# Optimization experiments

Measured on AMD Instinct MI355X. Metric: run time of the kernel, lower is better.

## Reference

```python
import jax, jax.numpy as jnp
import numpy as np

NUM_EXPERT = 16
IN_DIM = 1024
OUT_DIM = 3072
TOTAL_TOKENS = 16384  # tokens pre-grouped by expert, contiguous blocks


def setup_inputs() -> dict:
    key = jax.random.key(0)
    k1, k2, k3 = jax.random.split(key, 3)
    inp = jax.random.normal(k1, (TOTAL_TOKENS, IN_DIM), dtype=jnp.float32)
    # per-expert token counts (sum == TOTAL_TOKENS); even split here
    fwd_expert_count = jnp.full((NUM_EXPERT,), TOTAL_TOKENS // NUM_EXPERT, dtype=jnp.int64)
    scale = 1.0 / np.sqrt(IN_DIM)
    weight = jax.random.normal(k2, (NUM_EXPERT, OUT_DIM, IN_DIM), dtype=jnp.float32) * scale
    bias = jax.random.normal(k3, (NUM_EXPERT, OUT_DIM), dtype=jnp.float32) * scale
    return {"inp": inp, "fwd_expert_count": fwd_expert_count, "weight": weight, "bias": bias}


def reference(inp, fwd_expert_count, weight, bias):
    # Grouped GEMM: token block e (size fwd_expert_count[e]) uses expert e's
    # weight: y = x @ W_e^T + b_e.  Tokens are contiguous per expert, so
    # expert id per token = repeat(arange(E), counts).
    T = inp.shape[0]
    E = weight.shape[0]
    expert_id = jnp.repeat(jnp.arange(E), fwd_expert_count, total_repeat_length=T)  # [T]
    out = jnp.zeros((T, weight.shape[1]), dtype=inp.dtype)
    # small fixed structural loop over experts (E=16); each iter is a dense GEMM
    for e in range(E):
        ye = inp @ weight[e].T + bias[e]  # [T, out_dim]
        out = jnp.where((expert_id == e)[:, None], ye, out)
    return out
```

## Files before the change

### kernel.cpp

```cpp
#include <hip/hip_runtime.h>

typedef __attribute__((ext_vector_type(8))) _Float16 f16x8;
typedef __attribute__((ext_vector_type(2))) __fp16   fp16x2;
typedef __attribute__((ext_vector_type(4))) float    f32x4;

#define TT 16384
#define KD 1024
#define ND 3072
#define NE 16
#define ASZ (TT * KD)
#define WSZ (NE * ND * KD)
#define NEED_WS ((size_t)(ASZ + WSZ) * 2)

#define BM 256
#define BN 256
#define BK 64
#define NSTEP (KD / BK)
#define ROWB (BK * 2)

#define BAR() __builtin_amdgcn_s_barrier()
#define WAIT_VM(n) asm volatile("s_waitcnt vmcnt(" #n ")" ::: "memory")

__device__ __forceinline__ int swz(int row, int kbyte) {
    return row * ROWB + (kbyte ^ ((row & 7) << 4));
}

__device__ __forceinline__ int find_expert(const void* cntp, int row0) {
    const int* w = (const int*)cntp;
    int oddsum = 0;
    #pragma unroll
    for (int i = 1; i < 16; i += 2) oddsum |= w[i];
    int e = 0;
    long long cum = 0;
    if (oddsum == 0) {
        const long long* c = (const long long*)cntp;
        #pragma unroll
        for (int i = 0; i < NE; ++i) { if ((long long)row0 >= cum) e = i; cum += c[i]; }
    } else {
        #pragma unroll
        for (int i = 0; i < NE; ++i) { if ((long long)row0 >= cum) e = i; cum += w[i]; }
    }
    return e;
}

__device__ __forceinline__ void gl16(const void* g, void* l) {
    __builtin_amdgcn_global_load_lds(
        (const __attribute__((address_space(1))) unsigned int*)g,
        (__attribute__((address_space(3))) unsigned int*)l, 16, 0, 0);
}

__global__ __launch_bounds__(256) void cvt_kernel(const float* __restrict__ A,
                                                  const float* __restrict__ W,
                                                  _Float16* __restrict__ dst) {
    size_t i = ((size_t)blockIdx.x * 256 + threadIdx.x) * 8;
    const float* src = (i < (size_t)ASZ) ? (A + i) : (W + (i - ASZ));
    f32x4 v0 = *(const f32x4*)src;
    f32x4 v1 = *(const f32x4*)(src + 4);
    f16x8 h;
    h[0] = (_Float16)v0[0]; h[1] = (_Float16)v0[1];
    h[2] = (_Float16)v0[2]; h[3] = (_Float16)v0[3];
    h[4] = (_Float16)v1[0]; h[5] = (_Float16)v1[1];
    h[6] = (_Float16)v1[2]; h[7] = (_Float16)v1[3];
    *(f16x8*)(dst + i) = h;
}

__launch_bounds__(512, 2)
__global__ void gemm16(const _Float16* __restrict__ A16,
                       const void* __restrict__ cnt,
                       const _Float16* __restrict__ W16,
                       const float* __restrict__ bias,
                       float* __restrict__ Y) {
    __shared__ __align__(16) char lds[2][2][BM * ROWB];

    const int nwg = gridDim.x;
    const int bid0 = blockIdx.x;
    const int wgid = (bid0 & 7) * (nwg >> 3) + (bid0 >> 3);

    const int mt = wgid / (ND / BN);
    const int nt = wgid % (ND / BN);
    const int row0 = mt * BM;
    const int col0 = nt * BN;

    const int e = find_expert(cnt, row0);
    const _Float16* We = W16 + (size_t)e * ND * KD;

    const int tid = threadIdx.x;
    const int l = tid & 63;
    const int w = tid >> 6;
    const int wr = w >> 2;
    const int wc = w & 3;
    const int lr = l & 15;
    const int lk = l >> 4;

    const int laneoff = ((l & 7) * 16) ^ ((l >> 3) << 4);
    const char* gA = (const char*)A16 +
                     (size_t)(row0 + w * 32 + (l >> 3)) * (KD * 2) + laneoff;
    const char* gB = (const char*)We +
                     (size_t)(col0 + w * 32 + (l >> 3)) * (KD * 2) + laneoff;

    auto issue = [&](int t, int buf) {
        const char* a = gA + t * 128;
        const char* b = gB + t * 128;
        char* la = &lds[buf][0][w * 4096];
        char* lb = &lds[buf][1][w * 4096];
        #pragma unroll
        for (int i = 0; i < 4; ++i) {
            gl16(a + i * (8 * KD * 2), la + i * 1024);
            gl16(b + i * (8 * KD * 2), lb + i * 1024);
        }
    };

    f32x4 acc[8][4] = {};

    auto compute = [&](const char* As, const char* Bs) {
        #pragma unroll
        for (int kk = 0; kk < 2; ++kk) {
            f16x8 af[8], bf[4];
            #pragma unroll
            for (int m = 0; m < 8; ++m) {
                int r = wr * 128 + m * 16 + lr;
                af[m] = *(const f16x8*)&As[swz(r, kk * 64 + lk * 16)];
            }
            #pragma unroll
            for (int n = 0; n < 4; ++n) {
                int r = wc * 64 + n * 16 + lr;
                bf[n] = *(const f16x8*)&Bs[swz(r, kk * 64 + lk * 16)];
            }
            __builtin_amdgcn_s_setprio(1);
            #pragma unroll
            for (int m = 0; m < 8; ++m)
                #pragma unroll
                for (int n = 0; n < 4; ++n)
                    acc[m][n] = __builtin_amdgcn_mfma_f32_16x16x32_f16(
                        af[m], bf[n], acc[m][n], 0, 0, 0);
            __builtin_amdgcn_s_setprio(0);
        }
    };

    issue(0, 0);
    issue(1, 1);
    WAIT_VM(8);
    BAR();

    for (int t = 0; t < NSTEP; ++t) {
        const int buf = t & 1;
        compute(lds[buf][0], lds[buf][1]);
        BAR();
        if (t + 2 < NSTEP) {
            issue(t + 2, buf);
            WAIT_VM(8);
            BAR();
        } else if (t + 1 < NSTEP) {
            WAIT_VM(0);
            BAR();
        }
    }

    const int cb = col0 + wc * 64;
    const int rb0_ = row0 + wr * 128;
    float bv[4];
    #pragma unroll
    for (int n = 0; n < 4; ++n) bv[n] = bias[(size_t)e * ND + cb + n * 16 + lr];
    #pragma unroll
    for (int m = 0; m < 8; ++m) {
        #pragma unroll
        for (int j = 0; j < 4; ++j) {
            int r = rb0_ + m * 16 + lk * 4 + j;
            float* yp = Y + (size_t)r * ND + cb + lr;
            #pragma unroll
            for (int n = 0; n < 4; ++n)
                yp[n * 16] = acc[m][n][j] + bv[n];
        }
    }
}

__launch_bounds__(512, 2)
__global__ void fallback_gemm(const float* __restrict__ A,
                              const void* __restrict__ cnt,
                              const float* __restrict__ W,
                              const float* __restrict__ bias,
                              float* __restrict__ Y) {
    __shared__ __align__(16) char ldsbuf[2][2][BM * ROWB];

    const int nwg = gridDim.x;
    const int bid0 = blockIdx.x;
    const int wgid = (bid0 & 7) * (nwg >> 3) + (bid0 >> 3);

    const int mt = wgid / (ND / BN);
    const int nt = wgid % (ND / BN);
    const int row0 = mt * BM;
    const int col0 = nt * BN;

    const int e = find_expert(cnt, row0);
    const float* We = W + (size_t)e * ND * KD;

    const int tid = threadIdx.x;
    const int lane = tid & 63;
    const int w = tid >> 6;
    const int wr = w >> 2;
    const int wc = w & 3;
    const int lr = lane & 15;
    const int lk = lane >> 4;

    int soff[4];
    size_t aoff[4], boff[4];
    #pragma unroll
    for (int c = 0; c < 4; ++c) {
        int q = c * 512 + tid;
        int r = q >> 3;
        int kb = (q & 7) * 8;
        soff[c] = swz(r, kb * 2);
        aoff[c] = (size_t)(row0 + r) * KD + kb;
        boff[c] = (size_t)(col0 + r) * KD + kb;
    }

    f32x4 ra[4][2], rb[4][2];

    auto load_regs = [&](int ks) {
        const int k0 = ks * BK;
        #pragma unroll
        for (int c = 0; c < 4; ++c) {
            const float* ap = A + aoff[c] + k0;
            ra[c][0] = *(const f32x4*)ap;
            ra[c][1] = *(const f32x4*)(ap + 4);
            const float* bp = We + boff[c] + k0;
            rb[c][0] = *(const f32x4*)bp;
            rb[c][1] = *(const f32x4*)(bp + 4);
        }
    };

    auto write_lds = [&](int buf) {
        #pragma unroll
        for (int c = 0; c < 4; ++c) {
            union { f16x8 v; fp16x2 h[4]; } ua, ub;
            ua.h[0] = __builtin_amdgcn_cvt_pkrtz(ra[c][0][0], ra[c][0][1]);
            ua.h[1] = __builtin_amdgcn_cvt_pkrtz(ra[c][0][2], ra[c][0][3]);
            ua.h[2] = __builtin_amdgcn_cvt_pkrtz(ra[c][1][0], ra[c][1][1]);
            ua.h[3] = __builtin_amdgcn_cvt_pkrtz(ra[c][1][2], ra[c][1][3]);
            ub.h[0] = __builtin_amdgcn_cvt_pkrtz(rb[c][0][0], rb[c][0][1]);
            ub.h[1] = __builtin_amdgcn_cvt_pkrtz(rb[c][0][2], rb[c][0][3]);
            ub.h[2] = __builtin_amdgcn_cvt_pkrtz(rb[c][1][0], rb[c][1][1]);
            ub.h[3] = __builtin_amdgcn_cvt_pkrtz(rb[c][1][2], rb[c][1][3]);
            *(f16x8*)&ldsbuf[buf][0][soff[c]] = ua.v;
            *(f16x8*)&ldsbuf[buf][1][soff[c]] = ub.v;
        }
    };

    f32x4 acc[8][4] = {};

    auto compute = [&](const char* As, const char* Bs) {
        #pragma unroll
        for (int kk = 0; kk < 2; ++kk) {
            f16x8 af[8], bf[4];
            #pragma unroll
            for (int m = 0; m < 8; ++m) {
                int r = wr * 128 + m * 16 + lr;
                af[m] = *(const f16x8*)&As[swz(r, kk * 64 + lk * 16)];
            }
            #pragma unroll
            for (int n = 0; n < 4; ++n) {
                int r = wc * 64 + n * 16 + lr;
                bf[n] = *(const f16x8*)&Bs[swz(r, kk * 64 + lk * 16)];
            }
            #pragma unroll
            for (int m = 0; m < 8; ++m)
                #pragma unroll
                for (int n = 0; n < 4; ++n)
                    acc[m][n] = __builtin_amdgcn_mfma_f32_16x16x32_f16(
                        af[m], bf[n], acc[m][n], 0, 0, 0);
        }
    };

    load_regs(0);
    write_lds(0);
    __syncthreads();

    for (int t = 0; t < NSTEP; ++t) {
        const int buf = t & 1;
        if (t + 1 < NSTEP) load_regs(t + 1);
        compute(ldsbuf[buf][0], ldsbuf[buf][1]);
        __syncthreads();
        if (t + 1 < NSTEP) write_lds(buf ^ 1);
        __syncthreads();
    }

    const int cb = col0 + wc * 64;
    const int rb0_ = row0 + wr * 128;
    float bv[4];
    #pragma unroll
    for (int n = 0; n < 4; ++n) bv[n] = bias[(size_t)e * ND + cb + n * 16 + lr];
    #pragma unroll
    for (int m = 0; m < 8; ++m) {
        #pragma unroll
        for (int j = 0; j < 4; ++j) {
            int r = rb0_ + m * 16 + lk * 4 + j;
            float* yp = Y + (size_t)r * ND + cb + lr;
            #pragma unroll
            for (int n = 0; n < 4; ++n)
                yp[n * 16] = acc[m][n][j] + bv[n];
        }
    }
}

extern "C" void kernel_launch(void* const* d_in, const int* in_sizes, int n_in,
                              void* d_out, int out_size, void* d_ws, size_t ws_size,
                              hipStream_t stream) {
    const float* inp  = (const float*)d_in[0];
    const void*  cnt  = d_in[1];
    const float* wgt  = (const float*)d_in[2];
    const float* bias = (const float*)d_in[3];
    float* out = (float*)d_out;

    dim3 grid((TT / BM) * (ND / BN));
    dim3 block(512);

    if (ws_size >= NEED_WS) {
        _Float16* ws16 = (_Float16*)d_ws;
        cvt_kernel<<<dim3((ASZ + WSZ) / (8 * 256)), dim3(256), 0, stream>>>(inp, wgt, ws16);
        gemm16<<<grid, block, 0, stream>>>(ws16, cnt, ws16 + ASZ, bias, out);
    } else {
        fallback_gemm<<<grid, block, 0, stream>>>(inp, cnt, wgt, bias, out);
    }
}
```

Before: 205.9 us.

## Split per-tile compute into four barrier-synchronized phases with one-step prefetch

Each K tile's MFMA work is now split into four quadrant phases. Each phase loads its own A/B fragments from LDS, then hits a barrier, runs its MFMAs at raised priority, and hits another barrier, so waves move in lockstep and LDS reads alternate with math across the workgroup. Prefetch changes from two tiles ahead to one: the next tile's global-to-LDS loads are issued just before computing the current tile, with a single barrier per iteration. This adds many barriers per step and leaves less time to hide load latency, in exchange for the hoped-for better interleaving of LDS traffic and MFMA across waves.

```diff
diff --git a/kernel.cpp b/kernel.cpp
--- a/kernel.cpp
+++ b/kernel.cpp
@@ -64,6 +64,37 @@
     *(f16x8*)(dst + i) = h;
 }
 
+#define PHASE(As, Bs, MH, NH) do {                                          \
+    f16x8 af[2][4], bf[2][2];                                               \
+    _Pragma("unroll")                                                       \
+    for (int kk = 0; kk < 2; ++kk) {                                        \
+        _Pragma("unroll")                                                   \
+        for (int m = 0; m < 4; ++m) {                                       \
+            int r = wr * 128 + ((MH) * 4 + m) * 16 + lr;                    \
+            af[kk][m] = *(const f16x8*)&(As)[swz(r, kk * 64 + lk * 16)];    \
+        }                                                                   \
+        _Pragma("unroll")                                                   \
+        for (int n = 0; n < 2; ++n) {                                       \
+            int r = wc * 64 + ((NH) * 2 + n) * 16 + lr;                     \
+            bf[kk][n] = *(const f16x8*)&(Bs)[swz(r, kk * 64 + lk * 16)];    \
+        }                                                                   \
+    }                                                                       \
+    __builtin_amdgcn_s_barrier();                                           \
+    __builtin_amdgcn_s_setprio(1);                                          \
+    _Pragma("unroll")                                                       \
+    for (int kk = 0; kk < 2; ++kk)                                          \
+        _Pragma("unroll")                                                   \
+        for (int m = 0; m < 4; ++m)                                         \
+            _Pragma("unroll")                                               \
+            for (int n = 0; n < 2; ++n)                                     \
+                acc[(MH) * 4 + m][(NH) * 2 + n] =                           \
+                    __builtin_amdgcn_mfma_f32_16x16x32_f16(                 \
+                        af[kk][m], bf[kk][n],                               \
+                        acc[(MH) * 4 + m][(NH) * 2 + n], 0, 0, 0);          \
+    __builtin_amdgcn_s_setprio(0);                                          \
+    __builtin_amdgcn_s_barrier();                                           \
+} while (0)
+
 __launch_bounds__(512, 2)
 __global__ void gemm16(const _Float16* __restrict__ A16,
                        const void* __restrict__ cnt,
@@ -112,48 +143,24 @@
 
     f32x4 acc[8][4] = {};
 
-    auto compute = [&](const char* As, const char* Bs) {
-        #pragma unroll
-        for (int kk = 0; kk < 2; ++kk) {
-            f16x8 af[8], bf[4];
-            #pragma unroll
-            for (int m = 0; m < 8; ++m) {
-                int r = wr * 128 + m * 16 + lr;
-                af[m] = *(const f16x8*)&As[swz(r, kk * 64 + lk * 16)];
-            }
-            #pragma unroll
-            for (int n = 0; n < 4; ++n) {
-                int r = wc * 64 + n * 16 + lr;
-                bf[n] = *(const f16x8*)&Bs[swz(r, kk * 64 + lk * 16)];
-            }
-            __builtin_amdgcn_s_setprio(1);
-            #pragma unroll
-            for (int m = 0; m < 8; ++m)
-                #pragma unroll
-                for (int n = 0; n < 4; ++n)
-                    acc[m][n] = __builtin_amdgcn_mfma_f32_16x16x32_f16(
-                        af[m], bf[n], acc[m][n], 0, 0, 0);
-            __builtin_amdgcn_s_setprio(0);
-        }
-    };
-
     issue(0, 0);
-    issue(1, 1);
-    WAIT_VM(8);
-    BAR();
 
     for (int t = 0; t < NSTEP; ++t) {
         const int buf = t & 1;
-        compute(lds[buf][0], lds[buf][1]);
+        if (t + 1 < NSTEP) {
+            issue(t + 1, buf ^ 1);
+            WAIT_VM(8);
+        } else {
+            WAIT_VM(0);
+        }
         BAR();
-        if (t + 2 < NSTEP) {
-            issue(t + 2, buf);
-            WAIT_VM(8);
-            BAR();
-        } else if (t + 1 < NSTEP) {
-            WAIT_VM(0);
-            BAR();
-        }
+
+        const char* As = lds[buf][0];
+        const char* Bs = lds[buf][1];
+        PHASE(As, Bs, 0, 0);
+        PHASE(As, Bs, 0, 1);
+        PHASE(As, Bs, 1, 0);
+        PHASE(As, Bs, 1, 1);
     }
 
     const int cb = col0 + wc * 64;
```

Measured after the change: 224.1 us. +8.8%, slower.

## Shrink GEMM tile to 128x128 with 256 threads and single-buffered LDS

Applied to the files above, without the earlier changes.

Shrinks the fp16 grouped GEMM tile from 256x256 with 512 threads to 128x128 with 256 threads (4 waves, each computing a 64x64 sub-tile). It drops the double-buffered LDS prefetch pipeline and s_setprio in favour of one LDS buffer with a wait-then-compute loop, and raises the occupancy hint to 3 blocks per CU. The aim is more workgroups and occupancy to hide latency, at the cost of less data reuse per tile, more global traffic, and no overlap between loads and MFMA within a block. The fallback path keeps the old 256x256 tiling under separate FBM/FBN macros.

```diff
diff --git a/kernel.cpp b/kernel.cpp
--- a/kernel.cpp
+++ b/kernel.cpp
@@ -12,11 +12,12 @@
 #define WSZ (NE * ND * KD)
 #define NEED_WS ((size_t)(ASZ + WSZ) * 2)
 
-#define BM 256
-#define BN 256
+#define BM 128
+#define BN 128
 #define BK 64
 #define NSTEP (KD / BK)
 #define ROWB (BK * 2)
+#define NTHREADS 256
 
 #define BAR() __builtin_amdgcn_s_barrier()
 #define WAIT_VM(n) asm volatile("s_waitcnt vmcnt(" #n ")" ::: "memory")
@@ -64,13 +65,14 @@
     *(f16x8*)(dst + i) = h;
 }
 
-__launch_bounds__(512, 2)
+__launch_bounds__(NTHREADS, 3)
 __global__ void gemm16(const _Float16* __restrict__ A16,
                        const void* __restrict__ cnt,
                        const _Float16* __restrict__ W16,
                        const float* __restrict__ bias,
                        float* __restrict__ Y) {
-    __shared__ __align__(16) char lds[2][2][BM * ROWB];
+    __shared__ __align__(16) char As[BM * ROWB];
+    __shared__ __align__(16) char Bs[BN * ROWB];
 
     const int nwg = gridDim.x;
     const int bid0 = blockIdx.x;
@@ -87,8 +89,8 @@
     const int tid = threadIdx.x;
     const int l = tid & 63;
     const int w = tid >> 6;
-    const int wr = w >> 2;
-    const int wc = w & 3;
+    const int wr = w >> 1;
+    const int wc = w & 1;
     const int lr = l & 15;
     const int lk = l >> 4;
 
@@ -98,11 +100,11 @@
     const char* gB = (const char*)We +
                      (size_t)(col0 + w * 32 + (l >> 3)) * (KD * 2) + laneoff;
 
-    auto issue = [&](int t, int buf) {
+    auto issue = [&](int t) {
         const char* a = gA + t * 128;
         const char* b = gB + t * 128;
-        char* la = &lds[buf][0][w * 4096];
-        char* lb = &lds[buf][1][w * 4096];
+        char* la = &As[w * 4096];
+        char* lb = &Bs[w * 4096];
         #pragma unroll
         for (int i = 0; i < 4; ++i) {
             gl16(a + i * (8 * KD * 2), la + i * 1024);
@@ -110,15 +112,19 @@
         }
     };
 
-    f32x4 acc[8][4] = {};
-
-    auto compute = [&](const char* As, const char* Bs) {
+    f32x4 acc[4][4] = {};
+
+    issue(0);
+    for (int t = 0; t < NSTEP; ++t) {
+        WAIT_VM(0);
+        BAR();
+
         #pragma unroll
         for (int kk = 0; kk < 2; ++kk) {
-            f16x8 af[8], bf[4];
-            #pragma unroll
-            for (int m = 0; m < 8; ++m) {
-                int r = wr * 128 + m * 16 + lr;
+            f16x8 af[4], bf[4];
+            #pragma unroll
+            for (int m = 0; m < 4; ++m) {
+                int r = wr * 64 + m * 16 + lr;
                 af[m] = *(const f16x8*)&As[swz(r, kk * 64 + lk * 16)];
             }
             #pragma unroll
@@ -126,43 +132,25 @@
                 int r = wc * 64 + n * 16 + lr;
                 bf[n] = *(const f16x8*)&Bs[swz(r, kk * 64 + lk * 16)];
             }
-            __builtin_amdgcn_s_setprio(1);
-            #pragma unroll
-            for (int m = 0; m < 8; ++m)
+            #pragma unroll
+            for (int m = 0; m < 4; ++m)
                 #pragma unroll
                 for (int n = 0; n < 4; ++n)
                     acc[m][n] = __builtin_amdgcn_mfma_f32_16x16x32_f16(
                         af[m], bf[n], acc[m][n], 0, 0, 0);
-            __builtin_amdgcn_s_setprio(0);
-        }
-    };
-
-    issue(0, 0);
-    issue(1, 1);
-    WAIT_VM(8);
-    BAR();
-
-    for (int t = 0; t < NSTEP; ++t) {
-        const int buf = t & 1;
-        compute(lds[buf][0], lds[buf][1]);
+        }
+
         BAR();
-        if (t + 2 < NSTEP) {
-            issue(t + 2, buf);
-            WAIT_VM(8);
-            BAR();
-        } else if (t + 1 < NSTEP) {
-            WAIT_VM(0);
-            BAR();
-        }
+        if (t + 1 < NSTEP) issue(t + 1);
     }
 
     const int cb = col0 + wc * 64;
-    const int rb0_ = row0 + wr * 128;
+    const int rb0_ = row0 + wr * 64;
     float bv[4];
     #pragma unroll
     for (int n = 0; n < 4; ++n) bv[n] = bias[(size_t)e * ND + cb + n * 16 + lr];
     #pragma unroll
-    for (int m = 0; m < 8; ++m) {
+    for (int m = 0; m < 4; ++m) {
         #pragma unroll
         for (int j = 0; j < 4; ++j) {
             int r = rb0_ + m * 16 + lk * 4 + j;
@@ -174,22 +162,24 @@
     }
 }
 
+#define FBM 256
+#define FBN 256
 __launch_bounds__(512, 2)
 __global__ void fallback_gemm(const float* __restrict__ A,
                               const void* __restrict__ cnt,
                               const float* __restrict__ W,
                               const float* __restrict__ bias,
                               float* __restrict__ Y) {
-    __shared__ __align__(16) char ldsbuf[2][2][BM * ROWB];
+    __shared__ __align__(16) char ldsbuf[2][2][FBM * ROWB];
 
     const int nwg = gridDim.x;
     const int bid0 = blockIdx.x;
     const int wgid = (bid0 & 7) * (nwg >> 3) + (bid0 >> 3);
 
-    const int mt = wgid / (ND / BN);
-    const int nt = wgid % (ND / BN);
-    const int row0 = mt * BM;
-    const int col0 = nt * BN;
+    const int mt = wgid / (ND / FBN);
+    const int nt = wgid % (ND / FBN);
+    const int row0 = mt * FBM;
+    const int col0 = nt * FBN;
 
     const int e = find_expert(cnt, row0);
     const float* We = W + (size_t)e * ND * KD;
@@ -248,19 +238,19 @@
 
     f32x4 acc[8][4] = {};
 
-    auto compute = [&](const char* As, const char* Bs) {
+    auto compute = [&](const char* Asb, const char* Bsb) {
         #pragma unroll
         for (int kk = 0; kk < 2; ++kk) {
             f16x8 af[8], bf[4];
             #pragma unroll
             for (int m = 0; m < 8; ++m) {
                 int r = wr * 128 + m * 16 + lr;
-                af[m] = *(const f16x8*)&As[swz(r, kk * 64 + lk * 16)];
+                af[m] = *(const f16x8*)&Asb[swz(r, kk * 64 + lk * 16)];
             }
             #pragma unroll
             for (int n = 0; n < 4; ++n) {
                 int r = wc * 64 + n * 16 + lr;
-                bf[n] = *(const f16x8*)&Bs[swz(r, kk * 64 + lk * 16)];
+                bf[n] = *(const f16x8*)&Bsb[swz(r, kk * 64 + lk * 16)];
             }
             #pragma unroll
             for (int m = 0; m < 8; ++m)
@@ -311,14 +301,13 @@
     const float* bias = (const float*)d_in[3];
     float* out = (float*)d_out;
 
-    dim3 grid((TT / BM) * (ND / BN));
-    dim3 block(512);
-
     if (ws_size >= NEED_WS) {
         _Float16* ws16 = (_Float16*)d_ws;
         cvt_kernel<<<dim3((ASZ + WSZ) / (8 * 256)), dim3(256), 0, stream>>>(inp, wgt, ws16);
-        gemm16<<<grid, block, 0, stream>>>(ws16, cnt, ws16 + ASZ, bias, out);
+        dim3 grid((TT / BM) * (ND / BN));
+        gemm16<<<grid, dim3(NTHREADS), 0, stream>>>(ws16, cnt, ws16 + ASZ, bias, out);
     } else {
-        fallback_gemm<<<grid, block, 0, stream>>>(inp, cnt, wgt, bias, out);
-    }
-}
+        dim3 grid((TT / FBM) * (ND / FBN));
+        fallback_gemm<<<grid, dim3(512), 0, stream>>>(inp, cnt, wgt, bias, out);
+    }
+}
```

New measurement: 210.4 us. 2.2% more time.

## Split GEMM tile into four quadrants with staggered half-tile LDS staging

Applied to the files above, without the earlier changes.

Restructures the 256x256 GEMM main loop so A and B tiles are held as two 128-row halves with separate double-buffered slots, and each K-step runs four MFMA quadrants with global-to-LDS loads for the next steps interleaved between them. Each wave now owns a 64x32 sub-block per quadrant instead of a 128x64 block, so fragment registers per phase shrink and loads overlap compute at finer granularity. This aims to hide memory latency and cut register pressure, but adds many more barriers per K-step and re-reads B0/A fragments from LDS.

```diff
diff --git a/kernel.cpp b/kernel.cpp
--- a/kernel.cpp
+++ b/kernel.cpp
@@ -1,8 +1,8 @@
 #include <hip/hip_runtime.h>
 
-typedef __attribute__((ext_vector_type(8))) _Float16 f16x8;
-typedef __attribute__((ext_vector_type(2))) __fp16   fp16x2;
-typedef __attribute__((ext_vector_type(4))) float    f32x4;
+typedef __attribute__((ext_vector_type(8)))  _Float16 f16x8;
+typedef __attribute__((ext_vector_type(2)))  __fp16   fp16x2;
+typedef __attribute__((ext_vector_type(4)))  float    f32x4;
 
 #define TT 16384
 #define KD 1024
@@ -64,13 +64,25 @@
     *(f16x8*)(dst + i) = h;
 }
 
+#define MFMA_Q(MH, NH) do {                                                  \
+    _Pragma("unroll")                                                        \
+    for (int kk = 0; kk < 2; ++kk)                                           \
+        _Pragma("unroll")                                                    \
+        for (int m = 0; m < 4; ++m)                                          \
+            _Pragma("unroll")                                                \
+            for (int n = 0; n < 2; ++n)                                      \
+                acc[MH][NH][m][n] = __builtin_amdgcn_mfma_f32_16x16x32_f16(  \
+                    af[kk][m], bf[kk][n], acc[MH][NH][m][n], 0, 0, 0);       \
+} while (0)
+
 __launch_bounds__(512, 2)
 __global__ void gemm16(const _Float16* __restrict__ A16,
                        const void* __restrict__ cnt,
                        const _Float16* __restrict__ W16,
                        const float* __restrict__ bias,
                        float* __restrict__ Y) {
-    __shared__ __align__(16) char lds[2][2][BM * ROWB];
+    __shared__ __align__(16) char Aslot[2][2][128 * ROWB];
+    __shared__ __align__(16) char Bslot[2][2][128 * ROWB];
 
     const int nwg = gridDim.x;
     const int bid0 = blockIdx.x;
@@ -93,85 +105,116 @@
     const int lk = l >> 4;
 
     const int laneoff = ((l & 7) * 16) ^ ((l >> 3) << 4);
-    const char* gA = (const char*)A16 +
-                     (size_t)(row0 + w * 32 + (l >> 3)) * (KD * 2) + laneoff;
-    const char* gB = (const char*)We +
-                     (size_t)(col0 + w * 32 + (l >> 3)) * (KD * 2) + laneoff;
-
-    auto issue = [&](int t, int buf) {
-        const char* a = gA + t * 128;
-        const char* b = gB + t * 128;
-        char* la = &lds[buf][0][w * 4096];
-        char* lb = &lds[buf][1][w * 4096];
-        #pragma unroll
-        for (int i = 0; i < 4; ++i) {
-            gl16(a + i * (8 * KD * 2), la + i * 1024);
-            gl16(b + i * (8 * KD * 2), lb + i * 1024);
-        }
+    const size_t srcoff = (size_t)(w * 16 + (l >> 3)) * (KD * 2) + laneoff;
+
+    const char* gA0 = (const char*)A16 + (size_t)row0 * (KD * 2);
+    const char* gA1 = gA0 + (size_t)128 * (KD * 2);
+    const char* gB0 = (const char*)We + (size_t)col0 * (KD * 2);
+    const char* gB1 = gB0 + (size_t)128 * (KD * 2);
+
+    auto stage_half = [&](const char* ghalf, char* slot, int t) {
+        const char* s = ghalf + t * 128 + srcoff;
+        gl16(s,                slot + w * 2048);
+        gl16(s + 8 * (KD * 2), slot + w * 2048 + 1024);
     };
 
-    f32x4 acc[8][4] = {};
-
-    auto compute = [&](const char* As, const char* Bs) {
-        #pragma unroll
-        for (int kk = 0; kk < 2; ++kk) {
-            f16x8 af[8], bf[4];
-            #pragma unroll
-            for (int m = 0; m < 8; ++m) {
-                int r = wr * 128 + m * 16 + lr;
-                af[m] = *(const f16x8*)&As[swz(r, kk * 64 + lk * 16)];
-            }
-            #pragma unroll
-            for (int n = 0; n < 4; ++n) {
-                int r = wc * 64 + n * 16 + lr;
-                bf[n] = *(const f16x8*)&Bs[swz(r, kk * 64 + lk * 16)];
-            }
-            __builtin_amdgcn_s_setprio(1);
-            #pragma unroll
-            for (int m = 0; m < 8; ++m)
+    f32x4 acc[2][2][4][2] = {};
+
+    stage_half(gA0, &Aslot[0][0][0], 0);
+    stage_half(gB0, &Bslot[0][0][0], 0);
+    stage_half(gA1, &Aslot[1][0][0], 0);
+    stage_half(gB1, &Bslot[1][0][0], 0);
+    stage_half(gA0, &Aslot[0][1][0], 1);
+    stage_half(gB0, &Bslot[0][1][0], 1);
+    WAIT_VM(4);
+    BAR();
+
+    for (int t = 0; t < NSTEP; ++t) {
+        const int par = t & 1, nxt = par ^ 1;
+        const char* A0s = Aslot[0][par];
+        const char* A1s = Aslot[1][par];
+        const char* B0s = Bslot[0][par];
+        const char* B1s = Bslot[1][par];
+
+        f16x8 af[2][4], bf[2][2];
+
+        auto read_A = [&](const char* slot) {
+            #pragma unroll
+            for (int kk = 0; kk < 2; ++kk)
                 #pragma unroll
-                for (int n = 0; n < 4; ++n)
-                    acc[m][n] = __builtin_amdgcn_mfma_f32_16x16x32_f16(
-                        af[m], bf[n], acc[m][n], 0, 0, 0);
-            __builtin_amdgcn_s_setprio(0);
-        }
-    };
-
-    issue(0, 0);
-    issue(1, 1);
-    WAIT_VM(8);
-    BAR();
-
-    for (int t = 0; t < NSTEP; ++t) {
-        const int buf = t & 1;
-        compute(lds[buf][0], lds[buf][1]);
-        BAR();
-        if (t + 2 < NSTEP) {
-            issue(t + 2, buf);
-            WAIT_VM(8);
-            BAR();
-        } else if (t + 1 < NSTEP) {
-            WAIT_VM(0);
-            BAR();
-        }
-    }
-
-    const int cb = col0 + wc * 64;
-    const int rb0_ = row0 + wr * 128;
-    float bv[4];
-    #pragma unroll
-    for (int n = 0; n < 4; ++n) bv[n] = bias[(size_t)e * ND + cb + n * 16 + lr];
-    #pragma unroll
-    for (int m = 0; m < 8; ++m) {
-        #pragma unroll
-        for (int j = 0; j < 4; ++j) {
-            int r = rb0_ + m * 16 + lk * 4 + j;
-            float* yp = Y + (size_t)r * ND + cb + lr;
-            #pragma unroll
-            for (int n = 0; n < 4; ++n)
-                yp[n * 16] = acc[m][n][j] + bv[n];
-        }
-    }
+                for (int m = 0; m < 4; ++m) {
+                    int r = wr * 64 + m * 16 + lr;
+                    af[kk][m] = *(const f16x8*)&slot[swz(r, kk * 64 + lk * 16)];
+                }
+        };
+        auto read_B = [&](const char* slot) {
+            #pragma unroll
+            for (int kk = 0; kk < 2; ++kk)
+                #pragma unroll
+                for (int n = 0; n < 2; ++n) {
+                    int r = wc * 32 + n * 16 + lr;
+                    bf[kk][n] = *(const f16x8*)&slot[swz(r, kk * 64 + lk * 16)];
+                }
+        };
+
+        read_A(A0s);
+        read_B(B0s);
+        if (t + 1 < NSTEP) {
+            stage_half(gA1, &Aslot[1][nxt][0], t + 1);
+            stage_half(gB1, &Bslot[1][nxt][0], t + 1);
+        }
+        BAR();
+        __builtin_amdgcn_s_setprio(1);
+        MFMA_Q(0, 0);
+        __builtin_amdgcn_s_setprio(0);
+        BAR();
+
+        read_B(B1s);
+        if (t + 2 < NSTEP) stage_half(gA0, &Aslot[0][par][0], t + 2);
+        BAR();
+        __builtin_amdgcn_s_setprio(1);
+        MFMA_Q(0, 1);
+        __builtin_amdgcn_s_setprio(0);
+        BAR();
+
+        read_A(A1s);
+        read_B(B0s);
+        BAR();
+        __builtin_amdgcn_s_setprio(1);
+        MFMA_Q(1, 0);
+        __builtin_amdgcn_s_setprio(0);
+        BAR();
+
+        read_B(B1s);
+        if (t + 2 < NSTEP) stage_half(gB0, &Bslot[0][par][0], t + 2);
+        BAR();
+        __builtin_amdgcn_s_setprio(1);
+        MFMA_Q(1, 1);
+        __builtin_amdgcn_s_setprio(0);
+        if (t + 2 < NSTEP) { WAIT_VM(4); }
+        else if (t + 1 < NSTEP) { WAIT_VM(0); }
+        BAR();
+    }
+
+    float bv[2][2];
+    #pragma unroll
+    for (int nh = 0; nh < 2; ++nh)
+        #pragma unroll
+        for (int n = 0; n < 2; ++n)
+            bv[nh][n] = bias[(size_t)e * ND + col0 + nh * 128 + wc * 32 + n * 16 + lr];
+    #pragma unroll
+    for (int mh = 0; mh < 2; ++mh)
+        #pragma unroll
+        for (int nh = 0; nh < 2; ++nh)
+            #pragma unroll
+            for (int m = 0; m < 4; ++m)
+                #pragma unroll
+                for (int j = 0; j < 4; ++j) {
+                    int r = row0 + mh * 128 + wr * 64 + m * 16 + lk * 4 + j;
+                    float* yp = Y + (size_t)r * ND + col0 + nh * 128 + wc * 32 + lr;
+                    yp[0]  = acc[mh][nh][m][0][j] + bv[nh][0];
+                    yp[16] = acc[mh][nh][m][1][j] + bv[nh][1];
+                }
 }
 
 __launch_bounds__(512, 2)
@@ -248,19 +291,19 @@
 
     f32x4 acc[8][4] = {};
 
-    auto compute = [&](const char* As, const char* Bs) {
+    auto compute = [&](const char* Asb, const char* Bsb) {
         #pragma unroll
         for (int kk = 0; kk < 2; ++kk) {
             f16x8 af[8], bf[4];
             #pragma unroll
             for (int m = 0; m < 8; ++m) {
                 int r = wr * 128 + m * 16 + lr;
-                af[m] = *(const f16x8*)&As[swz(r, kk * 64 + lk * 16)];
+                af[m] = *(const f16x8*)&Asb[swz(r, kk * 64 + lk * 16)];
             }
             #pragma unroll
             for (int n = 0; n < 4; ++n) {
                 int r = wc * 64 + n * 16 + lr;
-                bf[n] = *(const f16x8*)&Bs[swz(r, kk * 64 + lk * 16)];
+                bf[n] = *(const f16x8*)&Bsb[swz(r, kk * 64 + lk * 16)];
             }
             #pragma unroll
             for (int m = 0; m < 8; ++m)
```

Result: slower. 224.0 us (+8.8%).
